# Optimization experiments

Hardware: AMD Instinct MI355X
Metric: run time of the kernel (lower is better)

## Reference

```python
import jax, jax.numpy as jnp
import numpy as np

B, N, E, H, GLOBAL_HEADS, LOCAL_K = 4, 2048, 512, 8, 1, 128
HD = E // H

def setup_inputs() -> dict:
    key = jax.random.key(0)
    ks = jax.random.split(key, 6)
    s = 0.02
    return {
        "x": jax.random.normal(ks[0], (B, N, E), dtype=jnp.float32),
        "attn_mask": jnp.ones((B, N), dtype=bool),
        "Wq": jax.random.normal(ks[1], (E, E), dtype=jnp.float32) * s,
        "bq": jnp.zeros((E,), dtype=jnp.float32),
        "Wk": jax.random.normal(ks[2], (E, E), dtype=jnp.float32) * s,
        "bk": jnp.zeros((E,), dtype=jnp.float32),
        "Wv": jax.random.normal(ks[3], (E, E), dtype=jnp.float32) * s,
        "bv": jnp.zeros((E,), dtype=jnp.float32),
        "Wo": jax.random.normal(ks[4], (E, E), dtype=jnp.float32) * s,
        "bo": jnp.zeros((E,), dtype=jnp.float32),
    }

def reference(x, attn_mask, Wq, bq, Wk, bk, Wv, bv, Wo, bo):
    scale = HD ** -0.5
    # projections (torch Linear: x @ W.T + b)
    q = (x @ Wq.T + bq).reshape(B, N, H, HD).transpose(0, 2, 1, 3)  # [B,H,N,HD]
    k = (x @ Wk.T + bk).reshape(B, N, H, HD).transpose(0, 2, 1, 3)
    v = (x @ Wv.T + bv).reshape(B, N, H, HD).transpose(0, 2, 1, 3)
    scores = jnp.einsum('bhid,bhjd->bhij', q, k) * scale  # [B,H,N,N]
    # per-head mask: first GLOBAL_HEADS heads full, rest banded |i-j|<=local_k
    idx = jnp.arange(N)
    local = jnp.abs(idx[:, None] - idx[None, :]) <= LOCAL_K  # [N,N]
    is_global = jnp.arange(H)[:, None, None] < GLOBAL_HEADS  # [H,1,1]
    head_mask = jnp.where(is_global, True, local[None, :, :])  # [H,N,N]
    allowed = head_mask[None] & attn_mask[:, None, None, :]  # [B,H,N,N]
    neg_inf = jnp.finfo(scores.dtype).min
    scores = jnp.where(allowed, scores, neg_inf)
    attn = jax.nn.softmax(scores, axis=-1)  # dropout p=0 (eval)
    out = jnp.einsum('bhij,bhjd->bhid', attn, v)  # [B,H,N,HD]
    out = out.transpose(0, 2, 1, 3).reshape(B, N, E)
    return out @ Wo.T + bo
```

## Files before the change

kernel.cpp:

```cpp
#include <hip/hip_runtime.h>
#include <hip/hip_bf16.h>

#define B_  4
#define N_  2048
#define E_  512
#define H_  8
#define HD_ 64
#define GH_ 1
#define LK_ 128
#define M_  (B_ * N_)
#define NCHUNK 4

typedef __attribute__((ext_vector_type(8))) short short8v;
typedef __attribute__((ext_vector_type(4))) short short4v;
typedef __attribute__((ext_vector_type(4))) float f32x4;

__device__ __forceinline__ unsigned short f2bf(float x) {
    unsigned u = __builtin_bit_cast(unsigned, x);
    return (unsigned short)((u + 0x7FFFu + ((u >> 16) & 1u)) >> 16);
}
__device__ __forceinline__ float bf2f(unsigned short h) {
    unsigned u = ((unsigned)h) << 16;
    return __builtin_bit_cast(float, u);
}
__device__ __forceinline__ void split4(const float* f, short4v& h, short4v& l) {
#pragma unroll
    for (int q = 0; q < 4; ++q) {
        unsigned short hb = f2bf(f[q]);
        h[q] = (short)hb;
        l[q] = (short)f2bf(f[q] - bf2f(hb));
    }
}

__device__ __forceinline__ void mfma_gemm_tile(const float* __restrict__ X,
                                               const float* __restrict__ W,
                                               const float* __restrict__ bias,
                                               float* __restrict__ C)
{
    __shared__ __align__(16) short sXh[128][40];
    __shared__ __align__(16) short sXl[128][40];
    __shared__ __align__(16) short sWh[128][40];
    __shared__ __align__(16) short sWl[128][40];

    const int t    = threadIdx.x;
    const int m0   = blockIdx.x * 128;
    const int j0   = blockIdx.y * 128;
    const int w    = t >> 6;
    const int lane = t & 63;
    const int wr   = w >> 1;
    const int wc   = w & 1;
    const int lr   = lane & 15;
    const int tr   = lane >> 4;

    f32x4 acc[4][4];
#pragma unroll
    for (int mt = 0; mt < 4; ++mt)
#pragma unroll
        for (int nt = 0; nt < 4; ++nt)
            acc[mt][nt] = (f32x4){0.f, 0.f, 0.f, 0.f};

    for (int k0 = 0; k0 < E_; k0 += 32) {
#pragma unroll
        for (int s = 0; s < 4; ++s) {
            int idx = t + s * 256;
            int row = idx >> 3;
            int c   = idx & 7;
            float4 xv = *(const float4*)&X[(size_t)(m0 + row) * E_ + k0 + c * 4];
            float4 wv = *(const float4*)&W[(size_t)(j0 + row) * E_ + k0 + c * 4];
            short4v xh, xl, wh, wl;
            float xf[4] = {xv.x, xv.y, xv.z, xv.w};
            float wf[4] = {wv.x, wv.y, wv.z, wv.w};
            split4(xf, xh, xl);
            split4(wf, wh, wl);
            *(short4v*)&sXh[row][c * 4] = xh;
            *(short4v*)&sXl[row][c * 4] = xl;
            *(short4v*)&sWh[row][c * 4] = wh;
            *(short4v*)&sWl[row][c * 4] = wl;
        }
        __syncthreads();

        short8v aH[4], aL[4], bH[4], bL[4];
#pragma unroll
        for (int mt = 0; mt < 4; ++mt) {
            int r = wr * 64 + mt * 16 + lr;
            aH[mt] = *(const short8v*)&sXh[r][tr * 8];
            aL[mt] = *(const short8v*)&sXl[r][tr * 8];
        }
#pragma unroll
        for (int nt = 0; nt < 4; ++nt) {
            int r = wc * 64 + nt * 16 + lr;
            bH[nt] = *(const short8v*)&sWh[r][tr * 8];
            bL[nt] = *(const short8v*)&sWl[r][tr * 8];
        }
#pragma unroll
        for (int mt = 0; mt < 4; ++mt)
#pragma unroll
            for (int nt = 0; nt < 4; ++nt) {
                acc[mt][nt] = __builtin_amdgcn_mfma_f32_16x16x32_bf16(aH[mt], bH[nt], acc[mt][nt], 0, 0, 0);
                acc[mt][nt] = __builtin_amdgcn_mfma_f32_16x16x32_bf16(aH[mt], bL[nt], acc[mt][nt], 0, 0, 0);
                acc[mt][nt] = __builtin_amdgcn_mfma_f32_16x16x32_bf16(aL[mt], bH[nt], acc[mt][nt], 0, 0, 0);
            }
        __syncthreads();
    }

#pragma unroll
    for (int mt = 0; mt < 4; ++mt)
#pragma unroll
        for (int nt = 0; nt < 4; ++nt) {
            int gcol = j0 + wc * 64 + nt * 16 + lr;
            float bv = bias[gcol];
#pragma unroll
            for (int i = 0; i < 4; ++i) {
                size_t grow = m0 + wr * 64 + mt * 16 + tr * 4 + i;
                C[grow * E_ + gcol] = acc[mt][nt][i] + bv;
            }
        }
}

__global__ __launch_bounds__(256) void proj_qkv_kernel(
    const float* __restrict__ x,
    const float* __restrict__ Wq, const float* __restrict__ bq,
    const float* __restrict__ Wk, const float* __restrict__ bk,
    const float* __restrict__ Wv, const float* __restrict__ bv,
    float* __restrict__ q, float* __restrict__ k, float* __restrict__ v)
{
    const float* W; const float* bias; float* C;
    if (blockIdx.z == 0)      { W = Wq; bias = bq; C = q; }
    else if (blockIdx.z == 1) { W = Wk; bias = bk; C = k; }
    else                      { W = Wv; bias = bv; C = v; }
    mfma_gemm_tile(x, W, bias, C);
}

__global__ __launch_bounds__(256) void out_proj_kernel(
    const float* __restrict__ ctx,
    const float* __restrict__ Wo, const float* __restrict__ bo,
    float* __restrict__ out)
{
    mfma_gemm_tile(ctx, Wo, bo, out);
}

__global__ __launch_bounds__(256) void attn_kernel(
    const float* __restrict__ q, const float* __restrict__ k,
    const float* __restrict__ v, float* __restrict__ ctx,
    float* __restrict__ Opart, float* __restrict__ mpart, float* __restrict__ lpart)
{
    __shared__ __align__(16) char smem_raw[55296];
    short (*sKh)[72]  = (short(*)[72])(smem_raw);
    short (*sKl)[72]  = (short(*)[72])(smem_raw + 9216);
    short (*sVTh)[72] = (short(*)[72])(smem_raw + 18432);
    short (*sVTl)[72] = (short(*)[72])(smem_raw + 27648);

    const int t    = threadIdx.x;
    const int w    = t >> 6;
    const int lane = t & 63;
    const int lo   = lane & 15;
    const int hi4  = lane >> 4;

    short (*sPh)[72] = (short(*)[72])(smem_raw + 36864 + w * 2304);
    short (*sPl)[72] = (short(*)[72])(smem_raw + 46080 + w * 2304);

    const int qb = blockIdx.x;
    const int gy = blockIdx.y;
    const int b  = blockIdx.z;
    const bool is_global = (gy < NCHUNK);
    const int h  = is_global ? 0 : (gy - NCHUNK + 1);
    const int q0 = qb * 64;
    const float scale = 0.125f;

    const float* qbase = q + (size_t)b * N_ * E_ + h * HD_;
    const float* kbase = k + (size_t)b * N_ * E_ + h * HD_;
    const float* vbase = v + (size_t)b * N_ * E_ + h * HD_;

    short8v qh[2], ql[2];
    {
        const float* qrow_p = qbase + (size_t)(q0 + w * 16 + lo) * E_;
#pragma unroll
        for (int ks = 0; ks < 2; ++ks) {
            float4 f0 = *(const float4*)&qrow_p[ks * 32 + hi4 * 8];
            float4 f1 = *(const float4*)&qrow_p[ks * 32 + hi4 * 8 + 4];
            float f[8] = {f0.x, f0.y, f0.z, f0.w, f1.x, f1.y, f1.z, f1.w};
#pragma unroll
            for (int j = 0; j < 8; ++j) {
                float sv = f[j] * scale;
                unsigned short hb = f2bf(sv);
                qh[ks][j] = (short)hb;
                ql[ks][j] = (short)f2bf(sv - bf2f(hb));
            }
        }
    }

    float m_[4] = {-1e30f, -1e30f, -1e30f, -1e30f};
    float l_[4] = {0.f, 0.f, 0.f, 0.f};
    f32x4 o[4];
#pragma unroll
    for (int f = 0; f < 4; ++f) o[f] = (f32x4){0.f, 0.f, 0.f, 0.f};

    int kb_lo, kb_hi;
    if (is_global) { kb_lo = gy * 8; kb_hi = gy * 8 + 7; }
    else {
        kb_lo = (qb - 2 > 0) ? qb - 2 : 0;
        kb_hi = (qb + 2 < N_ / 64 - 1) ? qb + 2 : N_ / 64 - 1;
    }

    for (int kb = kb_lo; kb <= kb_hi; ++kb) {
        const int k0 = kb * 64;
#pragma unroll
        for (int s = 0; s < 4; ++s) {
            int idx = t + s * 256;
            int row = idx >> 4;
            int c4  = (idx & 15) * 4;
            float4 kv = *(const float4*)&kbase[(size_t)(k0 + row) * E_ + c4];
            float f[4] = {kv.x, kv.y, kv.z, kv.w};
            short4v hh, ll;
            split4(f, hh, ll);
            *(short4v*)&sKh[row][c4] = hh;
            *(short4v*)&sKl[row][c4] = ll;
        }
        {
            int d0 = (t & 15) * 4;
            int kk = (t >> 4) * 4;
            float vs[4][4];
#pragma unroll
            for (int j = 0; j < 4; ++j) {
                float4 vv = *(const float4*)&vbase[(size_t)(k0 + kk + j) * E_ + d0];
                vs[j][0] = vv.x; vs[j][1] = vv.y; vs[j][2] = vv.z; vs[j][3] = vv.w;
            }
#pragma unroll
            for (int qd = 0; qd < 4; ++qd) {
                int row = d0 + qd;
                int swz = (row >> 2) & 7;
                int col = (kk & 7) | (((kk >> 3) ^ swz) << 3);
                short4v hh, ll;
#pragma unroll
                for (int j = 0; j < 4; ++j) {
                    unsigned short hb = f2bf(vs[j][qd]);
                    hh[j] = (short)hb;
                    ll[j] = (short)f2bf(vs[j][qd] - bf2f(hb));
                }
                *(short4v*)&sVTh[row][col] = hh;
                *(short4v*)&sVTl[row][col] = ll;
            }
        }
        __syncthreads();

        f32x4 s_[4];
#pragma unroll
        for (int f = 0; f < 4; ++f) s_[f] = (f32x4){0.f, 0.f, 0.f, 0.f};
#pragma unroll
        for (int ks = 0; ks < 2; ++ks) {
#pragma unroll
            for (int f = 0; f < 4; ++f) {
                short8v bh = *(const short8v*)&sKh[f * 16 + lo][ks * 32 + hi4 * 8];
                short8v bl = *(const short8v*)&sKl[f * 16 + lo][ks * 32 + hi4 * 8];
                s_[f] = __builtin_amdgcn_mfma_f32_16x16x32_bf16(qh[ks], bh, s_[f], 0, 0, 0);
                s_[f] = __builtin_amdgcn_mfma_f32_16x16x32_bf16(qh[ks], bl, s_[f], 0, 0, 0);
                s_[f] = __builtin_amdgcn_mfma_f32_16x16x32_bf16(ql[ks], bh, s_[f], 0, 0, 0);
            }
        }

        if (!is_global && (kb - qb == 2 || kb - qb == -2)) {
#pragma unroll
            for (int f = 0; f < 4; ++f)
#pragma unroll
                for (int i = 0; i < 4; ++i) {
                    int dd = (q0 + w * 16 + 4 * hi4 + i) - (k0 + f * 16 + lo);
                    if (dd > LK_ || dd < -LK_) s_[f][i] = -1e30f;
                }
        }

        float p[4][4], fold[4];
#pragma unroll
        for (int i = 0; i < 4; ++i) {
            float pm = fmaxf(fmaxf(s_[0][i], s_[1][i]), fmaxf(s_[2][i], s_[3][i]));
            pm = fmaxf(pm, __shfl_xor(pm, 1));
            pm = fmaxf(pm, __shfl_xor(pm, 2));
            pm = fmaxf(pm, __shfl_xor(pm, 4));
            pm = fmaxf(pm, __shfl_xor(pm, 8));
            float mn = fmaxf(m_[i], pm);
            fold[i] = __expf(m_[i] - mn);
            float ps = 0.f;
#pragma unroll
            for (int f = 0; f < 4; ++f) {
                p[f][i] = __expf(s_[f][i] - mn);
                ps += p[f][i];
            }
            ps += __shfl_xor(ps, 1);
            ps += __shfl_xor(ps, 2);
            ps += __shfl_xor(ps, 4);
            ps += __shfl_xor(ps, 8);
            l_[i] = l_[i] * fold[i] + ps;
            m_[i] = mn;
        }
#pragma unroll
        for (int f = 0; f < 4; ++f)
#pragma unroll
            for (int i = 0; i < 4; ++i) o[f][i] *= fold[i];

#pragma unroll
        for (int f = 0; f < 4; ++f)
#pragma unroll
            for (int i = 0; i < 4; ++i) {
                unsigned short hb = f2bf(p[f][i]);
                sPh[4 * hi4 + i][f * 16 + lo] = (short)hb;
                sPl[4 * hi4 + i][f * 16 + lo] = (short)f2bf(p[f][i] - bf2f(hb));
            }

#pragma unroll
        for (int ks = 0; ks < 2; ++ks) {
            short8v pah = *(const short8v*)&sPh[lo][ks * 32 + hi4 * 8];
            short8v pal = *(const short8v*)&sPl[lo][ks * 32 + hi4 * 8];
#pragma unroll
            for (int f = 0; f < 4; ++f) {
                int row = f * 16 + lo;
                int col = ((hi4 + 4 * ks) ^ ((row >> 2) & 7)) << 3;
                short8v bvh = *(const short8v*)&sVTh[row][col];
                short8v bvl = *(const short8v*)&sVTl[row][col];
                o[f] = __builtin_amdgcn_mfma_f32_16x16x32_bf16(pah, bvh, o[f], 0, 0, 0);
                o[f] = __builtin_amdgcn_mfma_f32_16x16x32_bf16(pah, bvl, o[f], 0, 0, 0);
                o[f] = __builtin_amdgcn_mfma_f32_16x16x32_bf16(pal, bvh, o[f], 0, 0, 0);
            }
        }
        __syncthreads();
    }

    if (is_global) {
#pragma unroll
        for (int f = 0; f < 4; ++f)
#pragma unroll
            for (int i = 0; i < 4; ++i) {
                size_t row = (size_t)(gy * B_ + b) * N_ + q0 + w * 16 + 4 * hi4 + i;
                Opart[row * HD_ + f * 16 + lo] = o[f][i];
            }
        if (lo == 0) {
#pragma unroll
            for (int i = 0; i < 4; ++i) {
                size_t idx = (size_t)(gy * B_ + b) * N_ + q0 + w * 16 + 4 * hi4 + i;
                mpart[idx] = m_[i];
                lpart[idx] = l_[i];
            }
        }
    } else {
        float invl[4];
#pragma unroll
        for (int i = 0; i < 4; ++i) invl[i] = 1.0f / l_[i];
#pragma unroll
        for (int f = 0; f < 4; ++f)
#pragma unroll
            for (int i = 0; i < 4; ++i) {
                size_t row = (size_t)b * N_ + q0 + w * 16 + 4 * hi4 + i;
                ctx[row * E_ + h * HD_ + f * 16 + lo] = o[f][i] * invl[i];
            }
    }
}

__global__ __launch_bounds__(256) void combine_kernel(
    const float* __restrict__ Opart, const float* __restrict__ mpart,
    const float* __restrict__ lpart, float* __restrict__ ctx)
{
    const int t   = threadIdx.x;
    const int row = blockIdx.x * 64 + (t & 63);
    const int dg  = t >> 6;

    float mc[NCHUNK], lc[NCHUNK];
    float M = -1e30f;
#pragma unroll
    for (int c = 0; c < NCHUNK; ++c) {
        size_t idx = (size_t)c * B_ * N_ + row;
        mc[c] = mpart[idx];
        lc[c] = lpart[idx];
        M = fmaxf(M, mc[c]);
    }
    float L = 0.0f, wgt[NCHUNK];
#pragma unroll
    for (int c = 0; c < NCHUNK; ++c) {
        wgt[c] = __expf(mc[c] - M);
        L += wgt[c] * lc[c];
    }
    float invL = 1.0f / L;

    float o[16] = {};
#pragma unroll
    for (int c = 0; c < NCHUNK; ++c) {
        const float4* op = (const float4*)(Opart + ((size_t)c * B_ * N_ + row) * HD_ + dg * 16);
        float wc_ = wgt[c];
#pragma unroll
        for (int c4 = 0; c4 < 4; ++c4) {
            float4 vv = op[c4];
            o[c4 * 4 + 0] += wc_ * vv.x; o[c4 * 4 + 1] += wc_ * vv.y;
            o[c4 * 4 + 2] += wc_ * vv.z; o[c4 * 4 + 3] += wc_ * vv.w;
        }
    }
    float* cb = ctx + (size_t)row * E_ +  dg * 16;
#pragma unroll
    for (int c4 = 0; c4 < 4; ++c4) {
        float4 w_;
        w_.x = o[c4 * 4 + 0] * invL; w_.y = o[c4 * 4 + 1] * invL;
        w_.z = o[c4 * 4 + 2] * invL; w_.w = o[c4 * 4 + 3] * invL;
        *(float4*)&cb[c4 * 4] = w_;
    }
}

extern "C" void kernel_launch(void* const* d_in, const int* in_sizes, int n_in,
                              void* d_out, int out_size, void* d_ws, size_t ws_size,
                              hipStream_t stream)
{
    const float* x  = (const float*)d_in[0];
    const float* Wq = (const float*)d_in[2];
    const float* bq = (const float*)d_in[3];
    const float* Wk = (const float*)d_in[4];
    const float* bk = (const float*)d_in[5];
    const float* Wv = (const float*)d_in[6];
    const float* bv = (const float*)d_in[7];
    const float* Wo = (const float*)d_in[8];
    const float* bo = (const float*)d_in[9];
    float* out = (float*)d_out;

    float* ws    = (float*)d_ws;
    float* q     = ws;
    float* k     = q     + (size_t)M_ * E_;
    float* v     = k     + (size_t)M_ * E_;
    float* ctx   = v     + (size_t)M_ * E_;
    float* Opart = ctx   + (size_t)M_ * E_;
    float* mpart = Opart + (size_t)NCHUNK * B_ * N_ * HD_;
    float* lpart = mpart + (size_t)NCHUNK * B_ * N_;

    dim3 gproj(M_ / 128, E_ / 128, 3);
    proj_qkv_kernel<<<gproj, 256, 0, stream>>>(x, Wq, bq, Wk, bk, Wv, bv, q, k, v);

    dim3 gattn(N_ / 64, NCHUNK + (H_ - GH_), B_);
    attn_kernel<<<gattn, 256, 0, stream>>>(q, k, v, ctx, Opart, mpart, lpart);

    combine_kernel<<<dim3(M_ / 64), 256, 0, stream>>>(Opart, mpart, lpart, ctx);

    dim3 gout(M_ / 128, E_ / 128, 1);
    out_proj_kernel<<<gout, 256, 0, stream>>>(ctx, Wo, bo, out);
}
```

Baseline: 246.5 us.

## Pre-split inputs and intermediates into bf16 hi/lo pairs stored head-major

Adds a prep kernel that splits x and all weights into bf16 hi/lo arrays once, and makes the QKV projection emit pre-scaled, pre-split q/k/v in a [B,H,N,HD] layout. Attention, combine and the output projection then read and write bf16 pairs instead of fp32. This removes the repeated per-tile float-to-bf16 splitting inside the GEMM and attention loops and turns strided per-head loads into contiguous ones. The cost is an extra launch, an extra pass over x, and scattered 2-byte stores in the projection epilogue. ctx reuses the x buffers.

After: 234.5 us. 4.9% less time.

```diff
diff --git a/kernel.cpp b/kernel.cpp
--- a/kernel.cpp
+++ b/kernel.cpp
@@ -32,10 +32,38 @@
     }
 }
 
-__device__ __forceinline__ void mfma_gemm_tile(const float* __restrict__ X,
-                                               const float* __restrict__ W,
-                                               const float* __restrict__ bias,
-                                               float* __restrict__ C)
+__global__ __launch_bounds__(256) void split_prep_kernel(
+    const float* __restrict__ x,  const float* __restrict__ Wq,
+    const float* __restrict__ Wk, const float* __restrict__ Wv,
+    const float* __restrict__ Wo,
+    short* __restrict__ xh,  short* __restrict__ xl,
+    short* __restrict__ wqh, short* __restrict__ wql,
+    short* __restrict__ wkh, short* __restrict__ wkl,
+    short* __restrict__ wvh, short* __restrict__ wvl,
+    short* __restrict__ woh, short* __restrict__ wol)
+{
+    const float* src; short* dh; short* dl; size_t n4;
+    switch (blockIdx.y) {
+        case 0:  src = x;  dh = xh;  dl = xl;  n4 = (size_t)M_ * E_ / 4; break;
+        case 1:  src = Wq; dh = wqh; dl = wql; n4 = (size_t)E_ * E_ / 4; break;
+        case 2:  src = Wk; dh = wkh; dl = wkl; n4 = (size_t)E_ * E_ / 4; break;
+        case 3:  src = Wv; dh = wvh; dl = wvl; n4 = (size_t)E_ * E_ / 4; break;
+        default: src = Wo; dh = woh; dl = wol; n4 = (size_t)E_ * E_ / 4; break;
+    }
+    size_t i = (size_t)blockIdx.x * 256 + threadIdx.x;
+    if (i >= n4) return;
+    float4 v = ((const float4*)src)[i];
+    float f[4] = {v.x, v.y, v.z, v.w};
+    short4v h, l;
+    split4(f, h, l);
+    ((short4v*)dh)[i] = h;
+    ((short4v*)dl)[i] = l;
+}
+
+__device__ __forceinline__ void gemm_bf16_acc(
+    const short* __restrict__ Xh, const short* __restrict__ Xl,
+    const short* __restrict__ Wh, const short* __restrict__ Wl,
+    int m0, int j0, f32x4 (&acc)[4][4])
 {
     __shared__ __align__(16) short sXh[128][40];
     __shared__ __align__(16) short sXl[128][40];
@@ -43,8 +71,6 @@
     __shared__ __align__(16) short sWl[128][40];
 
     const int t    = threadIdx.x;
-    const int m0   = blockIdx.x * 128;
-    const int j0   = blockIdx.y * 128;
     const int w    = t >> 6;
     const int lane = t & 63;
     const int wr   = w >> 1;
@@ -52,30 +78,16 @@
     const int lr   = lane & 15;
     const int tr   = lane >> 4;
 
-    f32x4 acc[4][4];
-#pragma unroll
-    for (int mt = 0; mt < 4; ++mt)
-#pragma unroll
-        for (int nt = 0; nt < 4; ++nt)
-            acc[mt][nt] = (f32x4){0.f, 0.f, 0.f, 0.f};
-
     for (int k0 = 0; k0 < E_; k0 += 32) {
 #pragma unroll
-        for (int s = 0; s < 4; ++s) {
+        for (int s = 0; s < 2; ++s) {
             int idx = t + s * 256;
-            int row = idx >> 3;
-            int c   = idx & 7;
-            float4 xv = *(const float4*)&X[(size_t)(m0 + row) * E_ + k0 + c * 4];
-            float4 wv = *(const float4*)&W[(size_t)(j0 + row) * E_ + k0 + c * 4];
-            short4v xh, xl, wh, wl;
-            float xf[4] = {xv.x, xv.y, xv.z, xv.w};
-            float wf[4] = {wv.x, wv.y, wv.z, wv.w};
-            split4(xf, xh, xl);
-            split4(wf, wh, wl);
-            *(short4v*)&sXh[row][c * 4] = xh;
-            *(short4v*)&sXl[row][c * 4] = xl;
-            *(short4v*)&sWh[row][c * 4] = wh;
-            *(short4v*)&sWl[row][c * 4] = wl;
+            int row = idx >> 2;
+            int c8  = (idx & 3) * 8;
+            *(short8v*)&sXh[row][c8] = *(const short8v*)&Xh[(size_t)(m0 + row) * E_ + k0 + c8];
+            *(short8v*)&sXl[row][c8] = *(const short8v*)&Xl[(size_t)(m0 + row) * E_ + k0 + c8];
+            *(short8v*)&sWh[row][c8] = *(const short8v*)&Wh[(size_t)(j0 + row) * E_ + k0 + c8];
+            *(short8v*)&sWl[row][c8] = *(const short8v*)&Wl[(size_t)(j0 + row) * E_ + k0 + c8];
         }
         __syncthreads();
 
@@ -102,46 +114,98 @@
             }
         __syncthreads();
     }
+}
+
+__global__ __launch_bounds__(256) void proj_qkv_kernel(
+    const short* __restrict__ xh,  const short* __restrict__ xl,
+    const short* __restrict__ wqh, const short* __restrict__ wql,
+    const short* __restrict__ wkh, const short* __restrict__ wkl,
+    const short* __restrict__ wvh, const short* __restrict__ wvl,
+    const float* __restrict__ bq,  const float* __restrict__ bk,
+    const float* __restrict__ bv,
+    short* __restrict__ qh, short* __restrict__ ql,
+    short* __restrict__ kh, short* __restrict__ kl,
+    short* __restrict__ vh, short* __restrict__ vl)
+{
+    const short *Wh, *Wl; const float* bias; short *dh, *dl; float scl;
+    if (blockIdx.z == 0)      { Wh = wqh; Wl = wql; bias = bq; dh = qh; dl = ql; scl = 0.125f; }
+    else if (blockIdx.z == 1) { Wh = wkh; Wl = wkl; bias = bk; dh = kh; dl = kl; scl = 1.0f; }
+    else                      { Wh = wvh; Wl = wvl; bias = bv; dh = vh; dl = vl; scl = 1.0f; }
+
+    const int m0 = blockIdx.x * 128;
+    const int j0 = blockIdx.y * 128;
+    const int t = threadIdx.x, w = t >> 6, lane = t & 63;
+    const int wr = w >> 1, wc = w & 1, lr = lane & 15, tr = lane >> 4;
+
+    f32x4 acc[4][4];
+#pragma unroll
+    for (int mt = 0; mt < 4; ++mt)
+#pragma unroll
+        for (int nt = 0; nt < 4; ++nt)
+            acc[mt][nt] = (f32x4){0.f, 0.f, 0.f, 0.f};
+
+    gemm_bf16_acc(xh, xl, Wh, Wl, m0, j0, acc);
 
 #pragma unroll
     for (int mt = 0; mt < 4; ++mt)
 #pragma unroll
         for (int nt = 0; nt < 4; ++nt) {
             int gcol = j0 + wc * 64 + nt * 16 + lr;
-            float bv = bias[gcol];
+            float bv_ = bias[gcol];
+            int hidx = gcol >> 6;
+            int d    = gcol & 63;
+#pragma unroll
+            for (int i = 0; i < 4; ++i) {
+                int grow = m0 + wr * 64 + mt * 16 + tr * 4 + i;
+                int bb = grow >> 11;
+                int nn = grow & 2047;
+                float val = (acc[mt][nt][i] + bv_) * scl;
+                size_t didx = (((size_t)bb * H_ + hidx) * N_ + nn) * HD_ + d;
+                unsigned short hb = f2bf(val);
+                dh[didx] = (short)hb;
+                dl[didx] = (short)f2bf(val - bf2f(hb));
+            }
+        }
+}
+
+__global__ __launch_bounds__(256) void out_proj_kernel(
+    const short* __restrict__ ctxh, const short* __restrict__ ctxl,
+    const short* __restrict__ woh,  const short* __restrict__ wol,
+    const float* __restrict__ bo,   float* __restrict__ out)
+{
+    const int m0 = blockIdx.x * 128;
+    const int j0 = blockIdx.y * 128;
+    const int t = threadIdx.x, w = t >> 6, lane = t & 63;
+    const int wr = w >> 1, wc = w & 1, lr = lane & 15, tr = lane >> 4;
+
+    f32x4 acc[4][4];
+#pragma unroll
+    for (int mt = 0; mt < 4; ++mt)
+#pragma unroll
+        for (int nt = 0; nt < 4; ++nt)
+            acc[mt][nt] = (f32x4){0.f, 0.f, 0.f, 0.f};
+
+    gemm_bf16_acc(ctxh, ctxl, woh, wol, m0, j0, acc);
+
+#pragma unroll
+    for (int mt = 0; mt < 4; ++mt)
+#pragma unroll
+        for (int nt = 0; nt < 4; ++nt) {
+            int gcol = j0 + wc * 64 + nt * 16 + lr;
+            float bv_ = bo[gcol];
 #pragma unroll
             for (int i = 0; i < 4; ++i) {
                 size_t grow = m0 + wr * 64 + mt * 16 + tr * 4 + i;
-                C[grow * E_ + gcol] = acc[mt][nt][i] + bv;
-            }
-        }
-}
-
-__global__ __launch_bounds__(256) void proj_qkv_kernel(
-    const float* __restrict__ x,
-    const float* __restrict__ Wq, const float* __restrict__ bq,
-    const float* __restrict__ Wk, const float* __restrict__ bk,
-    const float* __restrict__ Wv, const float* __restrict__ bv,
-    float* __restrict__ q, float* __restrict__ k, float* __restrict__ v)
-{
-    const float* W; const float* bias; float* C;
-    if (blockIdx.z == 0)      { W = Wq; bias = bq; C = q; }
-    else if (blockIdx.z == 1) { W = Wk; bias = bk; C = k; }
-    else                      { W = Wv; bias = bv; C = v; }
-    mfma_gemm_tile(x, W, bias, C);
-}
-
-__global__ __launch_bounds__(256) void out_proj_kernel(
-    const float* __restrict__ ctx,
-    const float* __restrict__ Wo, const float* __restrict__ bo,
-    float* __restrict__ out)
-{
-    mfma_gemm_tile(ctx, Wo, bo, out);
+                out[grow * E_ + gcol] = acc[mt][nt][i] + bv_;
+            }
+        }
 }
 
 __global__ __launch_bounds__(256) void attn_kernel(
-    const float* __restrict__ q, const float* __restrict__ k,
-    const float* __restrict__ v, float* __restrict__ ctx,
+    const short* __restrict__ qh, const short* __restrict__ ql,
+    const short* __restrict__ kh, const short* __restrict__ kl,
+    const short* __restrict__ vh, const short* __restrict__ vl,
+    short* __restrict__ ctxh, short* __restrict__ ctxl,
     float* __restrict__ Opart, float* __restrict__ mpart, float* __restrict__ lpart)
 {
     __shared__ __align__(16) char smem_raw[55296];
@@ -165,27 +229,16 @@
     const bool is_global = (gy < NCHUNK);
     const int h  = is_global ? 0 : (gy - NCHUNK + 1);
     const int q0 = qb * 64;
-    const float scale = 0.125f;
-
-    const float* qbase = q + (size_t)b * N_ * E_ + h * HD_;
-    const float* kbase = k + (size_t)b * N_ * E_ + h * HD_;
-    const float* vbase = v + (size_t)b * N_ * E_ + h * HD_;
-
-    short8v qh[2], ql[2];
+
+    const size_t hb_off = ((size_t)b * H_ + h) * N_ * HD_;
+
+    short8v qfh[2], qfl[2];
     {
-        const float* qrow_p = qbase + (size_t)(q0 + w * 16 + lo) * E_;
+        const size_t qrow = hb_off + (size_t)(q0 + w * 16 + lo) * HD_;
 #pragma unroll
         for (int ks = 0; ks < 2; ++ks) {
-            float4 f0 = *(const float4*)&qrow_p[ks * 32 + hi4 * 8];
-            float4 f1 = *(const float4*)&qrow_p[ks * 32 + hi4 * 8 + 4];
-            float f[8] = {f0.x, f0.y, f0.z, f0.w, f1.x, f1.y, f1.z, f1.w};
-#pragma unroll
-            for (int j = 0; j < 8; ++j) {
-                float sv = f[j] * scale;
-                unsigned short hb = f2bf(sv);
-                qh[ks][j] = (short)hb;
-                ql[ks][j] = (short)f2bf(sv - bf2f(hb));
-            }
+            qfh[ks] = *(const short8v*)&qh[qrow + ks * 32 + hi4 * 8];
+            qfl[ks] = *(const short8v*)&ql[qrow + ks * 32 + hi4 * 8];
         }
     }
 
@@ -205,40 +258,34 @@
     for (int kb = kb_lo; kb <= kb_hi; ++kb) {
         const int k0 = kb * 64;
 #pragma unroll
-        for (int s = 0; s < 4; ++s) {
+        for (int s = 0; s < 2; ++s) {
             int idx = t + s * 256;
-            int row = idx >> 4;
-            int c4  = (idx & 15) * 4;
-            float4 kv = *(const float4*)&kbase[(size_t)(k0 + row) * E_ + c4];
-            float f[4] = {kv.x, kv.y, kv.z, kv.w};
-            short4v hh, ll;
-            split4(f, hh, ll);
-            *(short4v*)&sKh[row][c4] = hh;
-            *(short4v*)&sKl[row][c4] = ll;
+            int row = idx >> 3;
+            int c8  = (idx & 7) * 8;
+            size_t src = hb_off + (size_t)(k0 + row) * HD_ + c8;
+            *(short8v*)&sKh[row][c8] = *(const short8v*)&kh[src];
+            *(short8v*)&sKl[row][c8] = *(const short8v*)&kl[src];
         }
         {
             int d0 = (t & 15) * 4;
             int kk = (t >> 4) * 4;
-            float vs[4][4];
+            short4v rh[4], rl[4];
 #pragma unroll
             for (int j = 0; j < 4; ++j) {
-                float4 vv = *(const float4*)&vbase[(size_t)(k0 + kk + j) * E_ + d0];
-                vs[j][0] = vv.x; vs[j][1] = vv.y; vs[j][2] = vv.z; vs[j][3] = vv.w;
+                size_t src = hb_off + (size_t)(k0 + kk + j) * HD_ + d0;
+                rh[j] = *(const short4v*)&vh[src];
+                rl[j] = *(const short4v*)&vl[src];
             }
 #pragma unroll
             for (int qd = 0; qd < 4; ++qd) {
                 int row = d0 + qd;
                 int swz = (row >> 2) & 7;
                 int col = (kk & 7) | (((kk >> 3) ^ swz) << 3);
-                short4v hh, ll;
-#pragma unroll
-                for (int j = 0; j < 4; ++j) {
-                    unsigned short hb = f2bf(vs[j][qd]);
-                    hh[j] = (short)hb;
-                    ll[j] = (short)f2bf(vs[j][qd] - bf2f(hb));
-                }
-                *(short4v*)&sVTh[row][col] = hh;
-                *(short4v*)&sVTl[row][col] = ll;
+                short4v th, tl;
+#pragma unroll
+                for (int j = 0; j < 4; ++j) { th[j] = rh[j][qd]; tl[j] = rl[j][qd]; }
+                *(short4v*)&sVTh[row][col] = th;
+                *(short4v*)&sVTl[row][col] = tl;
             }
         }
         __syncthreads();
@@ -252,9 +299,9 @@
             for (int f = 0; f < 4; ++f) {
                 short8v bh = *(const short8v*)&sKh[f * 16 + lo][ks * 32 + hi4 * 8];
                 short8v bl = *(const short8v*)&sKl[f * 16 + lo][ks * 32 + hi4 * 8];
-                s_[f] = __builtin_amdgcn_mfma_f32_16x16x32_bf16(qh[ks], bh, s_[f], 0, 0, 0);
-                s_[f] = __builtin_amdgcn_mfma_f32_16x16x32_bf16(qh[ks], bl, s_[f], 0, 0, 0);
-                s_[f] = __builtin_amdgcn_mfma_f32_16x16x32_bf16(ql[ks], bh, s_[f], 0, 0, 0);
+                s_[f] = __builtin_amdgcn_mfma_f32_16x16x32_bf16(qfh[ks], bh, s_[f], 0, 0, 0);
+                s_[f] = __builtin_amdgcn_mfma_f32_16x16x32_bf16(qfh[ks], bl, s_[f], 0, 0, 0);
+                s_[f] = __builtin_amdgcn_mfma_f32_16x16x32_bf16(qfl[ks], bh, s_[f], 0, 0, 0);
             }
         }
 
@@ -348,14 +395,19 @@
 #pragma unroll
             for (int i = 0; i < 4; ++i) {
                 size_t row = (size_t)b * N_ + q0 + w * 16 + 4 * hi4 + i;
-                ctx[row * E_ + h * HD_ + f * 16 + lo] = o[f][i] * invl[i];
+                float val = o[f][i] * invl[i];
+                size_t didx = row * E_ + h * HD_ + f * 16 + lo;
+                unsigned short hb = f2bf(val);
+                ctxh[didx] = (short)hb;
+                ctxl[didx] = (short)f2bf(val - bf2f(hb));
             }
     }
 }
 
 __global__ __launch_bounds__(256) void combine_kernel(
     const float* __restrict__ Opart, const float* __restrict__ mpart,
-    const float* __restrict__ lpart, float* __restrict__ ctx)
+    const float* __restrict__ lpart,
+    short* __restrict__ ctxh, short* __restrict__ ctxl)
 {
     const int t   = threadIdx.x;
     const int row = blockIdx.x * 64 + (t & 63);
@@ -390,13 +442,19 @@
             o[c4 * 4 + 2] += wc_ * vv.z; o[c4 * 4 + 3] += wc_ * vv.w;
         }
     }
-    float* cb = ctx + (size_t)row * E_ +  dg * 16;
 #pragma unroll
     for (int c4 = 0; c4 < 4; ++c4) {
-        float4 w_;
-        w_.x = o[c4 * 4 + 0] * invL; w_.y = o[c4 * 4 + 1] * invL;
-        w_.z = o[c4 * 4 + 2] * invL; w_.w = o[c4 * 4 + 3] * invL;
-        *(float4*)&cb[c4 * 4] = w_;
+        short4v hh, ll;
+#pragma unroll
+        for (int j = 0; j < 4; ++j) {
+            float val = o[c4 * 4 + j] * invL;
+            unsigned short hb = f2bf(val);
+            hh[j] = (short)hb;
+            ll[j] = (short)f2bf(val - bf2f(hb));
+        }
+        size_t didx = (size_t)row * E_ +  dg * 16 + c4 * 4;
+        *(short4v*)&ctxh[didx] = hh;
+        *(short4v*)&ctxl[didx] = ll;
     }
 }
 
@@ -415,23 +473,42 @@
     const float* bo = (const float*)d_in[9];
     float* out = (float*)d_out;
 
-    float* ws    = (float*)d_ws;
-    float* q     = ws;
-    float* k     = q     + (size_t)M_ * E_;
-    float* v     = k     + (size_t)M_ * E_;
-    float* ctx   = v     + (size_t)M_ * E_;
-    float* Opart = ctx   + (size_t)M_ * E_;
-    float* mpart = Opart + (size_t)NCHUNK * B_ * N_ * HD_;
-    float* lpart = mpart + (size_t)NCHUNK * B_ * N_;
-
-    dim3 gproj(M_ / 128, E_ / 128, 3);
-    proj_qkv_kernel<<<gproj, 256, 0, stream>>>(x, Wq, bq, Wk, bk, Wv, bv, q, k, v);
-
-    dim3 gattn(N_ / 64, NCHUNK + (H_ - GH_), B_);
-    attn_kernel<<<gattn, 256, 0, stream>>>(q, k, v, ctx, Opart, mpart, lpart);
-
-    combine_kernel<<<dim3(M_ / 64), 256, 0, stream>>>(Opart, mpart, lpart, ctx);
-
-    dim3 gout(M_ / 128, E_ / 128, 1);
-    out_proj_kernel<<<gout, 256, 0, stream>>>(ctx, Wo, bo, out);
-}
+    const size_t TS = (size_t)M_ * E_ * 2;
+    const size_t WS = (size_t)E_ * E_ * 2;
+    char* p = (char*)d_ws;
+    short* xh = (short*)p;            p += TS;
+    short* xl = (short*)p;            p += TS;
+    short* qh = (short*)p;            p += TS;
+    short* ql = (short*)p;            p += TS;
+    short* kh = (short*)p;            p += TS;
+    short* kl = (short*)p;            p += TS;
+    short* vh = (short*)p;            p += TS;
+    short* vl = (short*)p;            p += TS;
+    short* wqh = (short*)p;           p += WS;
+    short* wql = (short*)p;           p += WS;
+    short* wkh = (short*)p;           p += WS;
+    short* wkl = (short*)p;           p += WS;
+    short* wvh = (short*)p;           p += WS;
+    short* wvl = (short*)p;           p += WS;
+    short* woh = (short*)p;           p += WS;
+    short* wol = (short*)p;           p += WS;
+    float* Opart = (float*)p;         p += (size_t)NCHUNK * B_ * N_ * HD_ * 4;
+    float* mpart = (float*)p;         p += (size_t)NCHUNK * B_ * N_ * 4;
+    float* lpart = (float*)p;         p += (size_t)NCHUNK * B_ * N_ * 4;
+    short* ctxh = xh;
+    short* ctxl = xl;
+
+    split_prep_kernel<<<dim3(4096, 5), 256, 0, stream>>>(
+        x, Wq, Wk, Wv, Wo, xh, xl, wqh, wql, wkh, wkl, wvh, wvl, woh, wol);
+
+    proj_qkv_kernel<<<dim3(M_ / 128, E_ / 128, 3), 256, 0, stream>>>(
+        xh, xl, wqh, wql, wkh, wkl, wvh, wvl, bq, bk, bv, qh, ql, kh, kl, vh, vl);
+
+    attn_kernel<<<dim3(N_ / 64, NCHUNK + (H_ - GH_), B_), 256, 0, stream>>>(
+        qh, ql, kh, kl, vh, vl, ctxh, ctxl, Opart, mpart, lpart);
+
+    combine_kernel<<<dim3(M_ / 64), 256, 0, stream>>>(Opart, mpart, lpart, ctxh, ctxl);
+
+    out_proj_kernel<<<dim3(M_ / 128, E_ / 128), 256, 0, stream>>>(
+        ctxh, ctxl, woh, wol, bo, out);
+}
```
